# Performance work log

Hardware: AMD Instinct MI355X
Metric: run time of the kernel (lower is better)

## Reference

```python
import jax, jax.numpy as jnp
import numpy as np

B, S, D, H, R = 2, 2048, 1024, 16, 4
HD = D // H  # 64


def _linear_params(key, din, dout):
    k1, k2 = jax.random.split(key)
    bound = 1.0 / np.sqrt(din)
    w = jax.random.uniform(k1, (din, dout), jnp.float32, -bound, bound)
    b = jax.random.uniform(k2, (dout,), jnp.float32, -bound, bound)
    return w, b


def setup_inputs() -> dict:
    key = jax.random.key(0)
    ks = jax.random.split(key, 10)
    x = jax.random.normal(ks[0], (B, S, D), jnp.float32)
    wq_p, bq_p = _linear_params(ks[1], D, D)
    wk_p, bk_p = _linear_params(ks[2], D, D)
    wv_p, bv_p = _linear_params(ks[3], D, D)
    wo_p, bo_p = _linear_params(ks[4], D, D)
    wq_s, bq_s = _linear_params(ks[5], D, H * R)
    wk_s, bk_s = _linear_params(ks[6], D, H * R)
    wv_s, bv_s = _linear_params(ks[7], D, H * R)
    wo_s, bo_s = _linear_params(ks[8], H * R, D)
    w_cross = jnp.float32(-0.1)
    return {"x": x,
            "wq_p": wq_p, "bq_p": bq_p, "wk_p": wk_p, "bk_p": bk_p,
            "wv_p": wv_p, "bv_p": bv_p, "wo_p": wo_p, "bo_p": bo_p,
            "wq_s": wq_s, "bq_s": bq_s, "wk_s": wk_s, "bk_s": bk_s,
            "wv_s": wv_s, "bv_s": bv_s, "wo_s": wo_s, "bo_s": bo_s,
            "w_cross": w_cross}


def _mha(x, wq, bq, wk, bk, wv, bv, dh, scale):
    b, s, _ = x.shape
    q = (x @ wq + bq).reshape(b, s, H, dh)
    k = (x @ wk + bk).reshape(b, s, H, dh)
    v = (x @ wv + bv).reshape(b, s, H, dh)
    scores = jnp.einsum('bqhd,bkhd->bhqk', q, k) / scale
    attn = jax.nn.softmax(scores, axis=-1)
    out = jnp.einsum('bhqk,bkhd->bqhd', attn, v)
    return out.reshape(b, s, H * dh)


def reference(x, wq_p, bq_p, wk_p, bk_p, wv_p, bv_p, wo_p, bo_p,
              wq_s, bq_s, wk_s, bk_s, wv_s, bv_s, wo_s, bo_s, w_cross):
    primary = _mha(x, wq_p, bq_p, wk_p, bk_p, wv_p, bv_p, HD, np.sqrt(HD)) @ wo_p + bo_p
    secondary = _mha(x, wq_s, bq_s, wk_s, bk_s, wv_s, bv_s, R, np.sqrt(R)) @ wo_s + bo_s
    return primary + w_cross * secondary
```

## Files before the change

kernel.cpp:

```cpp
#include <hip/hip_runtime.h>
#include <stdint.h>

typedef unsigned short u16;
typedef __bf16 bf16x8 __attribute__((ext_vector_type(8)));
typedef float f32x4 __attribute__((ext_vector_type(4)));
typedef u16 u16x8 __attribute__((ext_vector_type(8)));
typedef u16 u16x4 __attribute__((ext_vector_type(4)));
typedef unsigned u32x4 __attribute__((ext_vector_type(4)));


__device__ __forceinline__ u16 f2bf(float f) {
  unsigned u = __builtin_bit_cast(unsigned, f);
  u += 0x7FFFu + ((u >> 16) & 1u);
  return (u16)(u >> 16);
}
__device__ __forceinline__ unsigned cvtpk(float lo, float hi) {
  unsigned r;
  asm("v_cvt_pk_bf16_f32 %0, %1, %2" : "=v"(r) : "v"(lo), "v"(hi));
  return r;
}
__device__ __forceinline__ void gld_lds16(const void* g, void* l) {
  __builtin_amdgcn_global_load_lds((__attribute__((address_space(1))) void*)(g),
                                   (__attribute__((address_space(3))) void*)(l),
                                   16, 0, 0);
}

__global__ __launch_bounds__(256)
void k_prep(const float* __restrict__ x,
            const float* __restrict__ wq_p, const float* __restrict__ wk_p,
            const float* __restrict__ wv_p, const float* __restrict__ wo_p,
            const float* __restrict__ wq_s, const float* __restrict__ wk_s,
            const float* __restrict__ wv_s, const float* __restrict__ wo_s,
            const float* __restrict__ bq_p, const float* __restrict__ bk_p,
            const float* __restrict__ bq_s, const float* __restrict__ bk_s,
            const float* __restrict__ bo_p, const float* __restrict__ bo_s,
            const float* __restrict__ wcr,
            u16* __restrict__ xb, u16* __restrict__ Wall, u16* __restrict__ Wvt,
            u16* __restrict__ Wvst, u16* __restrict__ Bto,
            float* __restrict__ ballqk, float* __restrict__ bfin) {
  const int id = blockIdx.x;
  if (id < 2048) {
    const int i = id * 256 + threadIdx.x;
    const float4* p = reinterpret_cast<const float4*>(x) + (size_t)i * 2;
    float4 a = p[0], b = p[1];
    u16x8 o;
    o[0] = f2bf(a.x); o[1] = f2bf(a.y); o[2] = f2bf(a.z); o[3] = f2bf(a.w);
    o[4] = f2bf(b.x); o[5] = f2bf(b.y); o[6] = f2bf(b.z); o[7] = f2bf(b.w);
    *reinterpret_cast<u16x8*>(xb + (size_t)i * 8) = o;
    return;
  }
  if (id < 6400) {
    __shared__ float tile[32][33];
    const int tx = threadIdx.x & 31, ty = threadIdx.x >> 5;
    const float* src; u16* dst; int N, ldd, n0, k0; float sc = 1.f;
    if (id < 6144) {
      const int tid = id - 2048, job = tid >> 10, t10 = tid & 1023;
      switch (job) {
        case 0: src = wq_p; dst = Wall;                       ldd = 1024; break;
        case 1: src = wk_p; dst = Wall + (size_t)1024 * 1024; ldd = 1024; break;
        case 2: src = wv_p; dst = Wvt;                        ldd = 1024; break;
        default: src = wo_p; dst = Bto;                       ldd = 1088; break;
      }
      N = 1024; n0 = (t10 & 31) * 32; k0 = (t10 >> 5) * 32;
    } else {
      const int tid = id - 6144, job = tid >> 6, t6 = tid & 63;
      int ntx;
      switch (job) {
        case 0: src = wq_s; dst = Wall + (size_t)2048 * 1024; N = 64;   ldd = 1024; ntx = 2; break;
        case 1: src = wk_s; dst = Wall + (size_t)2112 * 1024; N = 64;   ldd = 1024; ntx = 2; break;
        case 2: src = wv_s; dst = Wvst;                       N = 64;   ldd = 1024; ntx = 2; break;
        default: src = wo_s; dst = Bto + 1024;                N = 1024; ldd = 1088; ntx = 32; sc = wcr[0]; break;
      }
      n0 = (t6 % ntx) * 32; k0 = (t6 / ntx) * 32;
    }
    #pragma unroll
    for (int i = 0; i < 4; ++i)
      tile[ty + i * 8][tx] = src[(size_t)(k0 + ty + i * 8) * N + n0 + tx];
    __syncthreads();
    #pragma unroll
    for (int i = 0; i < 4; ++i)
      dst[(size_t)(n0 + ty + i * 8) * ldd + k0 + tx] = f2bf(tile[tx][ty + i * 8] * sc);
    return;
  }
  const int i = (id - 6400) * 256 + threadIdx.x;
  if (i < 1024)       ballqk[i] = bq_p[i];
  else if (i < 2048)  ballqk[i] = bk_p[i - 1024];
  else if (i < 2112)  ballqk[i] = bq_s[i - 2048];
  else if (i < 2176)  ballqk[i] = bk_s[i - 2112];
  if (i < 1024) bfin[i] = bo_p[i] + wcr[0] * bo_s[i];
}

template <int BN, int WAVES_M, int OUTMODE, int OHD>
__device__ __forceinline__
void gemm_body(const u16* __restrict__ A, int lda,
               const u16* __restrict__ Bt, int ldb,
               const float* __restrict__ bias,
               void* __restrict__ Cv, int ldc, int K,
               int bx, int by, u16* sm) {
  constexpr int WM = 128 / WAVES_M;
  constexpr int MF = WM / 16;
  u16* Atile = sm;
  u16* Btile = sm + 8192;
  const int t = threadIdx.x, w = t >> 6;
  const int lane = t & 63, l4 = lane & 15, g = lane >> 4;
  const int wr = (WAVES_M == 4) ? w : (w >> 1);
  const int wc = (WAVES_M == 4) ? 0 : (w & 1);
  const int m0 = bx * 128, n0 = by * BN;

  auto stage = [&](int buf, int kt) {
    const int k0 = kt * 32;
    #pragma unroll
    for (int r = 0; r < 2; ++r) {
      const int slot = r * 256 + t;
      const int row = slot >> 2, blk = slot & 3;
      const int srcb = blk ^ ((row >> 1) & 3);
      gld_lds16(A + (size_t)(m0 + row) * lda + k0 + srcb * 8,
                &Atile[buf * 4096 + (r * 256 + w * 64) * 8]);
    }
    #pragma unroll
    for (int r = 0; r < BN / 64; ++r) {
      const int slot = r * 256 + t;
      const int row = slot >> 2, blk = slot & 3;
      const int srcb = blk ^ ((row >> 1) & 3);
      gld_lds16(Bt + (size_t)(n0 + row) * ldb + k0 + srcb * 8,
                &Btile[buf * (BN * 32) + (r * 256 + w * 64) * 8]);
    }
  };

  const f32x4 vz = {0.f, 0.f, 0.f, 0.f};
  f32x4 acc[MF][4];
  #pragma unroll
  for (int mi = 0; mi < MF; ++mi)
    #pragma unroll
    for (int ni = 0; ni < 4; ++ni) acc[mi][ni] = vz;

  const int nkt = K >> 5;
  stage(0, 0);
  __syncthreads();
  for (int kt = 0; kt < nkt; ++kt) {
    const int cur = kt & 1;
    if (kt + 1 < nkt) stage(cur ^ 1, kt + 1);
    bf16x8 af[MF], bfv[4];
    #pragma unroll
    for (int mi = 0; mi < MF; ++mi) {
      const int row = wr * WM + mi * 16 + l4;
      const int blk = g ^ ((row >> 1) & 3);
      af[mi] = *reinterpret_cast<const bf16x8*>(&Atile[cur * 4096 + row * 32 + blk * 8]);
    }
    #pragma unroll
    for (int ni = 0; ni < 4; ++ni) {
      const int row = wc * 64 + ni * 16 + l4;
      const int blk = g ^ ((row >> 1) & 3);
      bfv[ni] = *reinterpret_cast<const bf16x8*>(&Btile[cur * (BN * 32) + row * 32 + blk * 8]);
    }
    #pragma unroll
    for (int mi = 0; mi < MF; ++mi)
      #pragma unroll
      for (int ni = 0; ni < 4; ++ni)
        acc[mi][ni] = __builtin_amdgcn_mfma_f32_16x16x32_bf16(af[mi], bfv[ni],
                                                              acc[mi][ni], 0, 0, 0);
    __syncthreads();
  }
  #pragma unroll
  for (int mi = 0; mi < MF; ++mi) {
    #pragma unroll
    for (int ni = 0; ni < 4; ++ni) {
      const int grow0 = m0 + wr * WM + mi * 16 + g * 4;
      const int gcol = n0 + wc * 64 + ni * 16 + l4;
      const float bb = bias ? bias[gcol] : 0.f;
      if constexpr (OUTMODE == 1) {
        const int bidx = grow0 >> 11, s0 = grow0 & 2047;
        const int hh = gcol / OHD, dd = gcol % OHD;
        u16x4 ov;
        #pragma unroll
        for (int r = 0; r < 4; ++r) ov[r] = f2bf(acc[mi][ni][r] + bb);
        *reinterpret_cast<u16x4*>((u16*)Cv +
            (size_t)((bidx * 16 + hh) * OHD + dd) * 2048 + s0) = ov;
      } else {
        #pragma unroll
        for (int r = 0; r < 4; ++r) {
          const float v = acc[mi][ni][r] + bb;
          if constexpr (OUTMODE == 0)
            ((u16*)Cv)[(size_t)(grow0 + r) * ldc + gcol] = f2bf(v);
          else
            ((float*)Cv)[(size_t)(grow0 + r) * ldc + gcol] = v;
        }
      }
    }
  }
}

__global__ __launch_bounds__(256, 2)
void k_proj3(const u16* __restrict__ xb, const u16* __restrict__ Wall,
             const u16* __restrict__ Wvt, const u16* __restrict__ Wvst,
             const float* __restrict__ ballqk, const float* __restrict__ bv_p,
             const float* __restrict__ bv_s,
             u16* __restrict__ QKs, u16* __restrict__ Vpt, u16* __restrict__ Vst) {
  __shared__ __attribute__((aligned(16))) u16 sm[16384];
  const int id = blockIdx.x;
  if (id < 544) {
    gemm_body<128, 2, 0, 64>(xb, 1024, Wall, 1024, ballqk, QKs, 2176, 1024,
                             id & 31, id >> 5, sm);
  } else if (id < 800) {
    const int lid = id - 544;
    gemm_body<128, 2, 1, 64>(xb, 1024, Wvt, 1024, bv_p, Vpt, 0, 1024,
                             lid & 31, lid >> 5, sm);
  } else {
    const int lid = id - 800;
    gemm_body<64, 4, 1, 4>(xb, 1024, Wvst, 1024, bv_s, Vst, 0, 1024,
                           lid & 31, lid >> 5, sm);
  }
}

__global__ __launch_bounds__(256, 2)
void k_gemm_final(const u16* __restrict__ A, const u16* __restrict__ Bt,
                  const float* __restrict__ bias, float* __restrict__ C) {
  __shared__ __attribute__((aligned(16))) u16 sm[16384];
  gemm_body<128, 2, 2, 64>(A, 1088, Bt, 1088, bias, C, 1024, 1088,
                           blockIdx.x, blockIdx.y, sm);
}

__global__ __launch_bounds__(256, 2)
void k_attn(const u16* __restrict__ QKs, const u16* __restrict__ Vpt,
            const u16* __restrict__ Vst, u16* __restrict__ Ao) {
  __shared__ __attribute__((aligned(16))) u16 sm[16416];
  const int t = threadIdx.x, w = t >> 6;
  const int lane = t & 63, l4 = lane & 15, g = lane >> 4;
  const int grp = blockIdx.x >> 3, sub = blockIdx.x & 7;

  if ((grp & 1) == 0) {
    u16* Klds = sm;
    u16* Vlds = sm + 8192;
    const int id = (grp >> 1) * 8 + sub;
    const int lin = (id & 7) * 64 + (id >> 3);
    const int qt = lin & 15, hb = lin >> 4;
    const int h = hb & 15, b = hb >> 4;
    const int q0 = qt * 128;

    const u16* Qbase = QKs + (size_t)(b * 2048 + q0) * 2176 + h * 64;
    const u16* Kbase = QKs + (size_t)(b * 2048) * 2176 + 1024 + h * 64;
    const u16* Vbase = Vpt + (size_t)((b * 16 + h) * 64) * 2048;

    #pragma unroll
    for (int r = 0; r < 2; ++r) {
      const int sl = r * 256 + t, row = sl >> 3, blk = sl & 7;
      const int srcb = blk ^ (row & 7);
      const int prow = (row & 32) | (((row >> 2) & 3) << 3) | (((row >> 4) & 1) << 2) | (row & 3);
      gld_lds16(Kbase + (size_t)prow * 2176 + srcb * 8, &Klds[(r * 256 + w * 64) * 8]);
      gld_lds16(Vbase + (size_t)row * 2048 + srcb * 8, &Vlds[(r * 256 + w * 64) * 8]);
    }

    bf16x8 aq[2][2];
    #pragma unroll
    for (int mi = 0; mi < 2; ++mi)
      #pragma unroll
      for (int kd = 0; kd < 2; ++kd)
        aq[mi][kd] = *reinterpret_cast<const bf16x8*>(
            Qbase + (size_t)(w * 32 + mi * 16 + l4) * 2176 + kd * 32 + g * 8);

    __syncthreads();

    const f32x4 vz = {0.f, 0.f, 0.f, 0.f};
    float l_r[2] = {0.f, 0.f};
    f32x4 acc_o[2][4];
    #pragma unroll
    for (int mi = 0; mi < 2; ++mi)
      #pragma unroll
      for (int nd = 0; nd < 4; ++nd) acc_o[mi][nd] = vz;

    for (int kt = 0; kt < 32; ++kt) {
      const int cur = kt & 1;
      if (kt < 31) {
        const int kn = kt + 1;
        #pragma unroll
        for (int r = 0; r < 2; ++r) {
          const int sl = r * 256 + t, row = sl >> 3, blk = sl & 7;
          const int srcb = blk ^ (row & 7);
          const int prow = (row & 32) | (((row >> 2) & 3) << 3) | (((row >> 4) & 1) << 2) | (row & 3);
          gld_lds16(Kbase + (size_t)(kn * 64 + prow) * 2176 + srcb * 8,
                    &Klds[(cur ^ 1) * 4096 + (r * 256 + w * 64) * 8]);
          gld_lds16(Vbase + (size_t)row * 2048 + kn * 64 + srcb * 8,
                    &Vlds[(cur ^ 1) * 4096 + (r * 256 + w * 64) * 8]);
        }
      }
      f32x4 sc[2][4];
      #pragma unroll
      for (int mi = 0; mi < 2; ++mi)
        #pragma unroll
        for (int ni = 0; ni < 4; ++ni) sc[mi][ni] = vz;
      #pragma unroll
      for (int kd = 0; kd < 2; ++kd) {
        bf16x8 bk[4];
        #pragma unroll
        for (int ni = 0; ni < 4; ++ni) {
          const int row = ni * 16 + l4;
          const int blk = (kd * 4 + g) ^ (row & 7);
          bk[ni] = *reinterpret_cast<const bf16x8*>(&Klds[cur * 4096 + row * 64 + blk * 8]);
        }
        __builtin_amdgcn_s_setprio(1);
        #pragma unroll
        for (int mi = 0; mi < 2; ++mi)
          #pragma unroll
          for (int ni = 0; ni < 4; ++ni)
            sc[mi][ni] = __builtin_amdgcn_mfma_f32_16x16x32_bf16(bk[ni], aq[mi][kd],
                                                                 sc[mi][ni], 0, 0, 0);
        __builtin_amdgcn_s_setprio(0);
      }
      unsigned pw[2][4][2];
      #pragma unroll
      for (int mi = 0; mi < 2; ++mi) {
        float rs = 0.f;
        #pragma unroll
        for (int ni = 0; ni < 4; ++ni) {
          const float a0 = __expf(sc[mi][ni][0] * 0.125f);
          const float a1 = __expf(sc[mi][ni][1] * 0.125f);
          const float a2 = __expf(sc[mi][ni][2] * 0.125f);
          const float a3 = __expf(sc[mi][ni][3] * 0.125f);
          rs += (a0 + a1) + (a2 + a3);
          pw[mi][ni][0] = cvtpk(a0, a1);
          pw[mi][ni][1] = cvtpk(a2, a3);
        }
        rs += __shfl_xor(rs, 16);
        rs += __shfl_xor(rs, 32);
        l_r[mi] += rs;
      }
      #pragma unroll
      for (int ks = 0; ks < 2; ++ks) {
        bf16x8 bv[4];
        #pragma unroll
        for (int nd = 0; nd < 4; ++nd) {
          const int row = nd * 16 + l4;
          const int blk = (ks * 4 + g) ^ (row & 7);
          bv[nd] = *reinterpret_cast<const bf16x8*>(&Vlds[cur * 4096 + row * 64 + blk * 8]);
        }
        __builtin_amdgcn_s_setprio(1);
        #pragma unroll
        for (int mi = 0; mi < 2; ++mi) {
          const u32x4 aw = {pw[mi][2 * ks][0], pw[mi][2 * ks][1],
                            pw[mi][2 * ks + 1][0], pw[mi][2 * ks + 1][1]};
          const bf16x8 ap = __builtin_bit_cast(bf16x8, aw);
          #pragma unroll
          for (int nd = 0; nd < 4; ++nd)
            acc_o[mi][nd] = __builtin_amdgcn_mfma_f32_16x16x32_bf16(ap, bv[nd],
                                                                    acc_o[mi][nd], 0, 0, 0);
        }
        __builtin_amdgcn_s_setprio(0);
      }
      __syncthreads();
    }
    float linv[2][4];
    #pragma unroll
    for (int mi = 0; mi < 2; ++mi)
      #pragma unroll
      for (int r = 0; r < 4; ++r) {
        const int src = (lane & 48) + ((lane & 48) >> 2) + r;
        linv[mi][r] = 1.0f / __shfl(l_r[mi], src);
      }
    #pragma unroll
    for (int mi = 0; mi < 2; ++mi)
      #pragma unroll
      for (int nd = 0; nd < 4; ++nd)
        #pragma unroll
        for (int r = 0; r < 4; ++r) {
          const int grow = b * 2048 + q0 + w * 32 + mi * 16 + g * 4 + r;
          const int gcol = h * 64 + nd * 16 + l4;
          Ao[(size_t)grow * 1088 + gcol] = f2bf(acc_o[mi][nd][r] * linv[mi][r]);
        }
    return;
  }

  u16* KsL = sm;
  u16* VtL = sm + 8192;
  const int sid = (grp >> 1) * 8 + sub;
  const int q0 = (sid & 15) * 128, h = (sid >> 4) & 15, b = sid >> 8;

  const u16* Vsrc = Vst + (size_t)((b * 16 + h) * 4) * 2048;
  #pragma unroll
  for (int r = 0; r < 4; ++r)
    gld_lds16(Vsrc + (size_t)r * 2048 + t * 8, &VtL[r * 2056 + w * 512]);
  #pragma unroll
  for (int i = 0; i < 8; ++i) {
    const int s = i * 256 + t;
    const uint2 kk = *reinterpret_cast<const uint2*>(
        QKs + (size_t)(b * 2048 + s) * 2176 + 2112 + h * 4);
    const int slot = (s & ~31) | (((s >> 2) & 1) << 4) | (((s >> 3) & 3) << 2) | (s & 3);
    *reinterpret_cast<uint2*>(&KsL[slot * 4]) = kk;
  }
  bf16x8 aq[2];
  #pragma unroll
  for (int mi = 0; mi < 2; ++mi) {
    u16x8 qv = {0, 0, 0, 0, 0, 0, 0, 0};
    if (g == 0) {
      const uint2 qq = *reinterpret_cast<const uint2*>(
          QKs + (size_t)(b * 2048 + q0 + w * 32 + mi * 16 + l4) * 2176 + 2048 + h * 4);
      qv[0] = (u16)(qq.x & 0xffff); qv[1] = (u16)(qq.x >> 16);
      qv[2] = (u16)(qq.y & 0xffff); qv[3] = (u16)(qq.y >> 16);
    }
    aq[mi] = __builtin_bit_cast(bf16x8, qv);
  }
  __syncthreads();

  const f32x4 vz = {0.f, 0.f, 0.f, 0.f};
  float l_r[2] = {0.f, 0.f};
  f32x4 acc[2];
  acc[0] = vz; acc[1] = vz;

  for (int kt = 0; kt < 32; ++kt) {
    bf16x8 bk[4];
    #pragma unroll
    for (int ni = 0; ni < 4; ++ni) {
      u16x8 kv = {0, 0, 0, 0, 0, 0, 0, 0};
      if (g == 0) {
        const uint2 kk = *reinterpret_cast<const uint2*>(
            &KsL[(kt * 64 + ni * 16 + l4) * 4]);
        kv[0] = (u16)(kk.x & 0xffff); kv[1] = (u16)(kk.x >> 16);
        kv[2] = (u16)(kk.y & 0xffff); kv[3] = (u16)(kk.y >> 16);
      }
      bk[ni] = __builtin_bit_cast(bf16x8, kv);
    }
    f32x4 sc[2][4];
    #pragma unroll
    for (int mi = 0; mi < 2; ++mi)
      #pragma unroll
      for (int ni = 0; ni < 4; ++ni)
        sc[mi][ni] = __builtin_amdgcn_mfma_f32_16x16x32_bf16(bk[ni], aq[mi], vz, 0, 0, 0);
    unsigned pw[2][4][2];
    #pragma unroll
    for (int mi = 0; mi < 2; ++mi) {
      float rs = 0.f;
      #pragma unroll
      for (int ni = 0; ni < 4; ++ni) {
        const float a0 = __expf(sc[mi][ni][0] * 0.5f);
        const float a1 = __expf(sc[mi][ni][1] * 0.5f);
        const float a2 = __expf(sc[mi][ni][2] * 0.5f);
        const float a3 = __expf(sc[mi][ni][3] * 0.5f);
        rs += (a0 + a1) + (a2 + a3);
        pw[mi][ni][0] = cvtpk(a0, a1);
        pw[mi][ni][1] = cvtpk(a2, a3);
      }
      rs += __shfl_xor(rs, 16);
      rs += __shfl_xor(rs, 32);
      l_r[mi] += rs;
    }
    #pragma unroll
    for (int ks = 0; ks < 2; ++ks) {
      const int blko = kt * 8 + ks * 4 + g;
      const int vrow = l4 & 3;
      const bf16x8 bv = *reinterpret_cast<const bf16x8*>(&VtL[vrow * 2056 + blko * 8]);
      #pragma unroll
      for (int mi = 0; mi < 2; ++mi) {
        const u32x4 aw = {pw[mi][2 * ks][0], pw[mi][2 * ks][1],
                          pw[mi][2 * ks + 1][0], pw[mi][2 * ks + 1][1]};
        const bf16x8 ap = __builtin_bit_cast(bf16x8, aw);
        acc[mi] = __builtin_amdgcn_mfma_f32_16x16x32_bf16(ap, bv, acc[mi], 0, 0, 0);
      }
    }
  }
  #pragma unroll
  for (int mi = 0; mi < 2; ++mi)
    #pragma unroll
    for (int r = 0; r < 4; ++r) {
      const int src = (lane & 48) + ((lane & 48) >> 2) + r;
      const float linv = 1.0f / __shfl(l_r[mi], src);
      if (l4 < 4) {
        const int grow = b * 2048 + q0 + w * 32 + mi * 16 + g * 4 + r;
        Ao[(size_t)grow * 1088 + 1024 + h * 4 + l4] = f2bf(acc[mi][r] * linv);
      }
    }
}

extern "C" void kernel_launch(void* const* d_in, const int* in_sizes, int n_in,
                              void* d_out, int out_size, void* d_ws, size_t ws_size,
                              hipStream_t stream) {
  (void)in_sizes; (void)n_in; (void)out_size; (void)ws_size;
  const float* x    = (const float*)d_in[0];
  const float* wq_p = (const float*)d_in[1];
  const float* bq_p = (const float*)d_in[2];
  const float* wk_p = (const float*)d_in[3];
  const float* bk_p = (const float*)d_in[4];
  const float* wv_p = (const float*)d_in[5];
  const float* bv_p = (const float*)d_in[6];
  const float* wo_p = (const float*)d_in[7];
  const float* bo_p = (const float*)d_in[8];
  const float* wq_s = (const float*)d_in[9];
  const float* bq_s = (const float*)d_in[10];
  const float* wk_s = (const float*)d_in[11];
  const float* bk_s = (const float*)d_in[12];
  const float* wv_s = (const float*)d_in[13];
  const float* bv_s = (const float*)d_in[14];
  const float* wo_s = (const float*)d_in[15];
  const float* bo_s = (const float*)d_in[16];
  const float* wcr  = (const float*)d_in[17];

  char* p = (char*)d_ws;
  auto take = [&](size_t bytes) { char* r = p; p += (bytes + 255) & ~(size_t)255; return r; };
  u16* xb      = (u16*)take((size_t)4096 * 1024 * 2);
  u16* Wall    = (u16*)take((size_t)2176 * 1024 * 2);
  u16* Wvt     = (u16*)take((size_t)1024 * 1024 * 2);
  u16* Wvst    = (u16*)take((size_t)64 * 1024 * 2);
  u16* Bto     = (u16*)take((size_t)1024 * 1088 * 2);
  float* ballqk= (float*)take(2176 * 4);
  float* bfin  = (float*)take(1024 * 4);
  u16* QKs     = (u16*)take((size_t)4096 * 2176 * 2);
  u16* Vpt     = (u16*)take((size_t)4096 * 1024 * 2);
  u16* Vst     = (u16*)take((size_t)2 * 16 * 4 * 2048 * 2);
  u16* Ao      = (u16*)take((size_t)4096 * 1088 * 2);

  k_prep<<<6409, 256, 0, stream>>>(x, wq_p, wk_p, wv_p, wo_p, wq_s, wk_s, wv_s, wo_s,
                                   bq_p, bk_p, bq_s, bk_s, bo_p, bo_s, wcr,
                                   xb, Wall, Wvt, Wvst, Bto, ballqk, bfin);

  k_proj3<<<832, 256, 0, stream>>>(xb, Wall, Wvt, Wvst, ballqk, bv_p, bv_s,
                                   QKs, Vpt, Vst);

  k_attn<<<1024, 256, 0, stream>>>(QKs, Vpt, Vst, Ao);

  k_gemm_final<<<dim3(32, 8), 256, 0, stream>>>(Ao, Bto, bfin, (float*)d_out);
}
```

Measured before the change: 152.7 us.

## Fuse primary and secondary attention into one block per query tile

Rather than using separate blocks for the head-dim-64 primary attention and the head-dim-4 secondary attention, each block now computes both for the same (batch, head, query tile). It shares the loop, the Q tile indexing and the barriers, and halves the grid from 1024 to 512 blocks. The goal is to hide the light secondary work inside the primary loop and to remove the imbalance between the two block types. In exchange, shared memory per block roughly doubles and register pressure rises, which may lower occupancy, and the smaller grid exposes less parallelism.

```diff
diff --git a/kernel.cpp b/kernel.cpp
--- a/kernel.cpp
+++ b/kernel.cpp
@@ -223,157 +223,31 @@
 __global__ __launch_bounds__(256, 2)
 void k_attn(const u16* __restrict__ QKs, const u16* __restrict__ Vpt,
             const u16* __restrict__ Vst, u16* __restrict__ Ao) {
-  __shared__ __attribute__((aligned(16))) u16 sm[16416];
+  __shared__ __attribute__((aligned(16))) u16 sm[32800];
+  u16* Klds = sm;
+  u16* Vlds = sm + 8192;
+  u16* KsL  = sm + 16384;
+  u16* VtL  = sm + 24576;
   const int t = threadIdx.x, w = t >> 6;
   const int lane = t & 63, l4 = lane & 15, g = lane >> 4;
-  const int grp = blockIdx.x >> 3, sub = blockIdx.x & 7;
-
-  if ((grp & 1) == 0) {
-    u16* Klds = sm;
-    u16* Vlds = sm + 8192;
-    const int id = (grp >> 1) * 8 + sub;
-    const int lin = (id & 7) * 64 + (id >> 3);
-    const int qt = lin & 15, hb = lin >> 4;
-    const int h = hb & 15, b = hb >> 4;
-    const int q0 = qt * 128;
-
-    const u16* Qbase = QKs + (size_t)(b * 2048 + q0) * 2176 + h * 64;
-    const u16* Kbase = QKs + (size_t)(b * 2048) * 2176 + 1024 + h * 64;
-    const u16* Vbase = Vpt + (size_t)((b * 16 + h) * 64) * 2048;
-
-    #pragma unroll
-    for (int r = 0; r < 2; ++r) {
-      const int sl = r * 256 + t, row = sl >> 3, blk = sl & 7;
-      const int srcb = blk ^ (row & 7);
-      const int prow = (row & 32) | (((row >> 2) & 3) << 3) | (((row >> 4) & 1) << 2) | (row & 3);
-      gld_lds16(Kbase + (size_t)prow * 2176 + srcb * 8, &Klds[(r * 256 + w * 64) * 8]);
-      gld_lds16(Vbase + (size_t)row * 2048 + srcb * 8, &Vlds[(r * 256 + w * 64) * 8]);
-    }
-
-    bf16x8 aq[2][2];
-    #pragma unroll
-    for (int mi = 0; mi < 2; ++mi)
-      #pragma unroll
-      for (int kd = 0; kd < 2; ++kd)
-        aq[mi][kd] = *reinterpret_cast<const bf16x8*>(
-            Qbase + (size_t)(w * 32 + mi * 16 + l4) * 2176 + kd * 32 + g * 8);
-
-    __syncthreads();
-
-    const f32x4 vz = {0.f, 0.f, 0.f, 0.f};
-    float l_r[2] = {0.f, 0.f};
-    f32x4 acc_o[2][4];
-    #pragma unroll
-    for (int mi = 0; mi < 2; ++mi)
-      #pragma unroll
-      for (int nd = 0; nd < 4; ++nd) acc_o[mi][nd] = vz;
-
-    for (int kt = 0; kt < 32; ++kt) {
-      const int cur = kt & 1;
-      if (kt < 31) {
-        const int kn = kt + 1;
-        #pragma unroll
-        for (int r = 0; r < 2; ++r) {
-          const int sl = r * 256 + t, row = sl >> 3, blk = sl & 7;
-          const int srcb = blk ^ (row & 7);
-          const int prow = (row & 32) | (((row >> 2) & 3) << 3) | (((row >> 4) & 1) << 2) | (row & 3);
-          gld_lds16(Kbase + (size_t)(kn * 64 + prow) * 2176 + srcb * 8,
-                    &Klds[(cur ^ 1) * 4096 + (r * 256 + w * 64) * 8]);
-          gld_lds16(Vbase + (size_t)row * 2048 + kn * 64 + srcb * 8,
-                    &Vlds[(cur ^ 1) * 4096 + (r * 256 + w * 64) * 8]);
-        }
-      }
-      f32x4 sc[2][4];
-      #pragma unroll
-      for (int mi = 0; mi < 2; ++mi)
-        #pragma unroll
-        for (int ni = 0; ni < 4; ++ni) sc[mi][ni] = vz;
-      #pragma unroll
-      for (int kd = 0; kd < 2; ++kd) {
-        bf16x8 bk[4];
-        #pragma unroll
-        for (int ni = 0; ni < 4; ++ni) {
-          const int row = ni * 16 + l4;
-          const int blk = (kd * 4 + g) ^ (row & 7);
-          bk[ni] = *reinterpret_cast<const bf16x8*>(&Klds[cur * 4096 + row * 64 + blk * 8]);
-        }
-        __builtin_amdgcn_s_setprio(1);
-        #pragma unroll
-        for (int mi = 0; mi < 2; ++mi)
-          #pragma unroll
-          for (int ni = 0; ni < 4; ++ni)
-            sc[mi][ni] = __builtin_amdgcn_mfma_f32_16x16x32_bf16(bk[ni], aq[mi][kd],
-                                                                 sc[mi][ni], 0, 0, 0);
-        __builtin_amdgcn_s_setprio(0);
-      }
-      unsigned pw[2][4][2];
-      #pragma unroll
-      for (int mi = 0; mi < 2; ++mi) {
-        float rs = 0.f;
-        #pragma unroll
-        for (int ni = 0; ni < 4; ++ni) {
-          const float a0 = __expf(sc[mi][ni][0] * 0.125f);
-          const float a1 = __expf(sc[mi][ni][1] * 0.125f);
-          const float a2 = __expf(sc[mi][ni][2] * 0.125f);
-          const float a3 = __expf(sc[mi][ni][3] * 0.125f);
-          rs += (a0 + a1) + (a2 + a3);
-          pw[mi][ni][0] = cvtpk(a0, a1);
-          pw[mi][ni][1] = cvtpk(a2, a3);
-        }
-        rs += __shfl_xor(rs, 16);
-        rs += __shfl_xor(rs, 32);
-        l_r[mi] += rs;
-      }
-      #pragma unroll
-      for (int ks = 0; ks < 2; ++ks) {
-        bf16x8 bv[4];
-        #pragma unroll
-        for (int nd = 0; nd < 4; ++nd) {
-          const int row = nd * 16 + l4;
-          const int blk = (ks * 4 + g) ^ (row & 7);
-          bv[nd] = *reinterpret_cast<const bf16x8*>(&Vlds[cur * 4096 + row * 64 + blk * 8]);
-        }
-        __builtin_amdgcn_s_setprio(1);
-        #pragma unroll
-        for (int mi = 0; mi < 2; ++mi) {
-          const u32x4 aw = {pw[mi][2 * ks][0], pw[mi][2 * ks][1],
-                            pw[mi][2 * ks + 1][0], pw[mi][2 * ks + 1][1]};
-          const bf16x8 ap = __builtin_bit_cast(bf16x8, aw);
-          #pragma unroll
-          for (int nd = 0; nd < 4; ++nd)
-            acc_o[mi][nd] = __builtin_amdgcn_mfma_f32_16x16x32_bf16(ap, bv[nd],
-                                                                    acc_o[mi][nd], 0, 0, 0);
-        }
-        __builtin_amdgcn_s_setprio(0);
-      }
-      __syncthreads();
-    }
-    float linv[2][4];
-    #pragma unroll
-    for (int mi = 0; mi < 2; ++mi)
-      #pragma unroll
-      for (int r = 0; r < 4; ++r) {
-        const int src = (lane & 48) + ((lane & 48) >> 2) + r;
-        linv[mi][r] = 1.0f / __shfl(l_r[mi], src);
-      }
-    #pragma unroll
-    for (int mi = 0; mi < 2; ++mi)
-      #pragma unroll
-      for (int nd = 0; nd < 4; ++nd)
-        #pragma unroll
-        for (int r = 0; r < 4; ++r) {
-          const int grow = b * 2048 + q0 + w * 32 + mi * 16 + g * 4 + r;
-          const int gcol = h * 64 + nd * 16 + l4;
-          Ao[(size_t)grow * 1088 + gcol] = f2bf(acc_o[mi][nd][r] * linv[mi][r]);
-        }
-    return;
-  }
-
-  u16* KsL = sm;
-  u16* VtL = sm + 8192;
-  const int sid = (grp >> 1) * 8 + sub;
-  const int q0 = (sid & 15) * 128, h = (sid >> 4) & 15, b = sid >> 8;
-
+  const int id = blockIdx.x;
+  const int lin = (id & 7) * 64 + (id >> 3);
+  const int qt = lin & 15, hb = lin >> 4;
+  const int h = hb & 15, b = hb >> 4;
+  const int q0 = qt * 128;
+
+  const u16* Qbase = QKs + (size_t)(b * 2048 + q0) * 2176 + h * 64;
+  const u16* Kbase = QKs + (size_t)(b * 2048) * 2176 + 1024 + h * 64;
+  const u16* Vbase = Vpt + (size_t)((b * 16 + h) * 64) * 2048;
+
+  #pragma unroll
+  for (int r = 0; r < 2; ++r) {
+    const int sl = r * 256 + t, row = sl >> 3, blk = sl & 7;
+    const int srcb = blk ^ (row & 7);
+    const int prow = (row & 32) | (((row >> 2) & 3) << 3) | (((row >> 4) & 1) << 2) | (row & 3);
+    gld_lds16(Kbase + (size_t)prow * 2176 + srcb * 8, &Klds[(r * 256 + w * 64) * 8]);
+    gld_lds16(Vbase + (size_t)row * 2048 + srcb * 8, &Vlds[(r * 256 + w * 64) * 8]);
+  }
   const u16* Vsrc = Vst + (size_t)((b * 16 + h) * 4) * 2048;
   #pragma unroll
   for (int r = 0; r < 4; ++r)
@@ -386,7 +260,14 @@
     const int slot = (s & ~31) | (((s >> 2) & 1) << 4) | (((s >> 3) & 3) << 2) | (s & 3);
     *reinterpret_cast<uint2*>(&KsL[slot * 4]) = kk;
   }
-  bf16x8 aq[2];
+  bf16x8 aq[2][2];
+  #pragma unroll
+  for (int mi = 0; mi < 2; ++mi)
+    #pragma unroll
+    for (int kd = 0; kd < 2; ++kd)
+      aq[mi][kd] = *reinterpret_cast<const bf16x8*>(
+          Qbase + (size_t)(w * 32 + mi * 16 + l4) * 2176 + kd * 32 + g * 8);
+  bf16x8 aqs[2];
   #pragma unroll
   for (int mi = 0; mi < 2; ++mi) {
     u16x8 qv = {0, 0, 0, 0, 0, 0, 0, 0};
@@ -396,44 +277,90 @@
       qv[0] = (u16)(qq.x & 0xffff); qv[1] = (u16)(qq.x >> 16);
       qv[2] = (u16)(qq.y & 0xffff); qv[3] = (u16)(qq.y >> 16);
     }
-    aq[mi] = __builtin_bit_cast(bf16x8, qv);
+    aqs[mi] = __builtin_bit_cast(bf16x8, qv);
   }
   __syncthreads();
 
   const f32x4 vz = {0.f, 0.f, 0.f, 0.f};
   float l_r[2] = {0.f, 0.f};
-  f32x4 acc[2];
-  acc[0] = vz; acc[1] = vz;
+  float l_rs[2] = {0.f, 0.f};
+  f32x4 acc_o[2][4];
+  f32x4 accs[2];
+  #pragma unroll
+  for (int mi = 0; mi < 2; ++mi) {
+    #pragma unroll
+    for (int nd = 0; nd < 4; ++nd) acc_o[mi][nd] = vz;
+    accs[mi] = vz;
+  }
 
   for (int kt = 0; kt < 32; ++kt) {
-    bf16x8 bk[4];
-    #pragma unroll
-    for (int ni = 0; ni < 4; ++ni) {
-      u16x8 kv = {0, 0, 0, 0, 0, 0, 0, 0};
-      if (g == 0) {
-        const uint2 kk = *reinterpret_cast<const uint2*>(
-            &KsL[(kt * 64 + ni * 16 + l4) * 4]);
-        kv[0] = (u16)(kk.x & 0xffff); kv[1] = (u16)(kk.x >> 16);
-        kv[2] = (u16)(kk.y & 0xffff); kv[3] = (u16)(kk.y >> 16);
-      }
-      bk[ni] = __builtin_bit_cast(bf16x8, kv);
+    const int cur = kt & 1;
+    if (kt < 31) {
+      const int kn = kt + 1;
+      #pragma unroll
+      for (int r = 0; r < 2; ++r) {
+        const int sl = r * 256 + t, row = sl >> 3, blk = sl & 7;
+        const int srcb = blk ^ (row & 7);
+        const int prow = (row & 32) | (((row >> 2) & 3) << 3) | (((row >> 4) & 1) << 2) | (row & 3);
+        gld_lds16(Kbase + (size_t)(kn * 64 + prow) * 2176 + srcb * 8,
+                  &Klds[(cur ^ 1) * 4096 + (r * 256 + w * 64) * 8]);
+        gld_lds16(Vbase + (size_t)row * 2048 + kn * 64 + srcb * 8,
+                  &Vlds[(cur ^ 1) * 4096 + (r * 256 + w * 64) * 8]);
+      }
     }
     f32x4 sc[2][4];
     #pragma unroll
     for (int mi = 0; mi < 2; ++mi)
       #pragma unroll
-      for (int ni = 0; ni < 4; ++ni)
-        sc[mi][ni] = __builtin_amdgcn_mfma_f32_16x16x32_bf16(bk[ni], aq[mi], vz, 0, 0, 0);
+      for (int ni = 0; ni < 4; ++ni) sc[mi][ni] = vz;
+    #pragma unroll
+    for (int kd = 0; kd < 2; ++kd) {
+      bf16x8 bk[4];
+      #pragma unroll
+      for (int ni = 0; ni < 4; ++ni) {
+        const int row = ni * 16 + l4;
+        const int blk = (kd * 4 + g) ^ (row & 7);
+        bk[ni] = *reinterpret_cast<const bf16x8*>(&Klds[cur * 4096 + row * 64 + blk * 8]);
+      }
+      __builtin_amdgcn_s_setprio(1);
+      #pragma unroll
+      for (int mi = 0; mi < 2; ++mi)
+        #pragma unroll
+        for (int ni = 0; ni < 4; ++ni)
+          sc[mi][ni] = __builtin_amdgcn_mfma_f32_16x16x32_bf16(bk[ni], aq[mi][kd],
+                                                               sc[mi][ni], 0, 0, 0);
+      __builtin_amdgcn_s_setprio(0);
+    }
+    f32x4 scs[2][4];
+    {
+      bf16x8 bks[4];
+      #pragma unroll
+      for (int ni = 0; ni < 4; ++ni) {
+        u16x8 kv = {0, 0, 0, 0, 0, 0, 0, 0};
+        if (g == 0) {
+          const uint2 kk = *reinterpret_cast<const uint2*>(
+              &KsL[(kt * 64 + ni * 16 + l4) * 4]);
+          kv[0] = (u16)(kk.x & 0xffff); kv[1] = (u16)(kk.x >> 16);
+          kv[2] = (u16)(kk.y & 0xffff); kv[3] = (u16)(kk.y >> 16);
+        }
+        bks[ni] = __builtin_bit_cast(bf16x8, kv);
+      }
+      #pragma unroll
+      for (int mi = 0; mi < 2; ++mi)
+        #pragma unroll
+        for (int ni = 0; ni < 4; ++ni)
+          scs[mi][ni] = __builtin_amdgcn_mfma_f32_16x16x32_bf16(bks[ni], aqs[mi], vz, 0, 0, 0);
+    }
     unsigned pw[2][4][2];
     #pragma unroll
     for (int mi = 0; mi < 2; ++mi) {
       float rs = 0.f;
       #pragma unroll
       for (int ni = 0; ni < 4; ++ni) {
-        const float a0 = __expf(sc[mi][ni][0] * 0.5f);
-        const float a1 = __expf(sc[mi][ni][1] * 0.5f);
-        const float a2 = __expf(sc[mi][ni][2] * 0.5f);
-        const float a3 = __expf(sc[mi][ni][3] * 0.5f);
+        const float a0 = __expf(sc[mi][ni][0] * 0.125f);
+        const float a1 = __expf(sc[mi][ni][1] * 0.125f);
+        const float a2 = __expf(sc[mi][ni][2] * 0.125f);
+        const float a3 = __expf(sc[mi][ni][3] * 0.125f);
         rs += (a0 + a1) + (a2 + a3);
         pw[mi][ni][0] = cvtpk(a0, a1);
         pw[mi][ni][1] = cvtpk(a2, a3);
@@ -442,29 +369,88 @@
       rs += __shfl_xor(rs, 32);
       l_r[mi] += rs;
     }
+    unsigned pws[2][4][2];
+    #pragma unroll
+    for (int mi = 0; mi < 2; ++mi) {
+      float rs = 0.f;
+      #pragma unroll
+      for (int ni = 0; ni < 4; ++ni) {
+        const float a0 = __expf(scs[mi][ni][0] * 0.5f);
+        const float a1 = __expf(scs[mi][ni][1] * 0.5f);
+        const float a2 = __expf(scs[mi][ni][2] * 0.5f);
+        const float a3 = __expf(scs[mi][ni][3] * 0.5f);
+        rs += (a0 + a1) + (a2 + a3);
+        pws[mi][ni][0] = cvtpk(a0, a1);
+        pws[mi][ni][1] = cvtpk(a2, a3);
+      }
+      rs += __shfl_xor(rs, 16);
+      rs += __shfl_xor(rs, 32);
+      l_rs[mi] += rs;
+    }
     #pragma unroll
     for (int ks = 0; ks < 2; ++ks) {
-      const int blko = kt * 8 + ks * 4 + g;
-      const int vrow = l4 & 3;
-      const bf16x8 bv = *reinterpret_cast<const bf16x8*>(&VtL[vrow * 2056 + blko * 8]);
+      bf16x8 bv[4];
+      #pragma unroll
+      for (int nd = 0; nd < 4; ++nd) {
+        const int row = nd * 16 + l4;
+        const int blk = (ks * 4 + g) ^ (row & 7);
+        bv[nd] = *reinterpret_cast<const bf16x8*>(&Vlds[cur * 4096 + row * 64 + blk * 8]);
+      }
+      __builtin_amdgcn_s_setprio(1);
       #pragma unroll
       for (int mi = 0; mi < 2; ++mi) {
         const u32x4 aw = {pw[mi][2 * ks][0], pw[mi][2 * ks][1],
                           pw[mi][2 * ks + 1][0], pw[mi][2 * ks + 1][1]};
         const bf16x8 ap = __builtin_bit_cast(bf16x8, aw);
-        acc[mi] = __builtin_amdgcn_mfma_f32_16x16x32_bf16(ap, bv, acc[mi], 0, 0, 0);
-      }
-    }
-  }
+        #pragma unroll
+        for (int nd = 0; nd < 4; ++nd)
+          acc_o[mi][nd] = __builtin_amdgcn_mfma_f32_16x16x32_bf16(ap, bv[nd],
+                                                                  acc_o[mi][nd], 0, 0, 0);
+      }
+      __builtin_amdgcn_s_setprio(0);
+    }
+    #pragma unroll
+    for (int ks = 0; ks < 2; ++ks) {
+      const int blko = kt * 8 + ks * 4 + g;
+      const int vrow = l4 & 3;
+      const bf16x8 bvs = *reinterpret_cast<const bf16x8*>(&VtL[vrow * 2056 + blko * 8]);
+      #pragma unroll
+      for (int mi = 0; mi < 2; ++mi) {
+        const u32x4 aw = {pws[mi][2 * ks][0], pws[mi][2 * ks][1],
+                          pws[mi][2 * ks + 1][0], pws[mi][2 * ks + 1][1]};
+        const bf16x8 ap = __builtin_bit_cast(bf16x8, aw);
+        accs[mi] = __builtin_amdgcn_mfma_f32_16x16x32_bf16(ap, bvs, accs[mi], 0, 0, 0);
+      }
+    }
+    __syncthreads();
+  }
+  float linv[2][4];
   #pragma unroll
   for (int mi = 0; mi < 2; ++mi)
     #pragma unroll
     for (int r = 0; r < 4; ++r) {
       const int src = (lane & 48) + ((lane & 48) >> 2) + r;
-      const float linv = 1.0f / __shfl(l_r[mi], src);
+      linv[mi][r] = 1.0f / __shfl(l_r[mi], src);
+    }
+  #pragma unroll
+  for (int mi = 0; mi < 2; ++mi)
+    #pragma unroll
+    for (int nd = 0; nd < 4; ++nd)
+      #pragma unroll
+      for (int r = 0; r < 4; ++r) {
+        const int grow = b * 2048 + q0 + w * 32 + mi * 16 + g * 4 + r;
+        const int gcol = h * 64 + nd * 16 + l4;
+        Ao[(size_t)grow * 1088 + gcol] = f2bf(acc_o[mi][nd][r] * linv[mi][r]);
+      }
+  #pragma unroll
+  for (int mi = 0; mi < 2; ++mi)
+    #pragma unroll
+    for (int r = 0; r < 4; ++r) {
+      const int src = (lane & 48) + ((lane & 48) >> 2) + r;
+      const float li = 1.0f / __shfl(l_rs[mi], src);
       if (l4 < 4) {
         const int grow = b * 2048 + q0 + w * 32 + mi * 16 + g * 4 + r;
-        Ao[(size_t)grow * 1088 + 1024 + h * 4 + l4] = f2bf(acc[mi][r] * linv);
+        Ao[(size_t)grow * 1088 + 1024 + h * 4 + l4] = f2bf(accs[mi][r] * li);
       }
     }
 }
@@ -513,7 +499,7 @@
   k_proj3<<<832, 256, 0, stream>>>(xb, Wall, Wvt, Wvst, ballqk, bv_p, bv_s,
                                    QKs, Vpt, Vst);
 
-  k_attn<<<1024, 256, 0, stream>>>(QKs, Vpt, Vst, Ao);
+  k_attn<<<512, 256, 0, stream>>>(QKs, Vpt, Vst, Ao);
 
   k_gemm_final<<<dim3(32, 8), 256, 0, stream>>>(Ao, Bto, bfin, (float*)d_out);
 }
```

Result: no change. 154.2 us (+0.9%).
